# Kernel optimization log

Measured on AMD Instinct MI355X. Metric: run time of the kernel, lower is better.

## Reference

```python
import jax, jax.numpy as jnp
import numpy as np

N = 100000
F_IN = 128
HID = 128
NCLS = 40
NEG_SLOPE = 0.2
BN_EPS = 1e-5


def setup_inputs() -> dict:
    key = jax.random.key(0)
    ks = jax.random.split(key, 16)
    x = jax.random.normal(ks[0], (N, F_IN), dtype=jnp.float32)
    # self-loop-free random edges: dst = (src + 1 + r) % N
    E = 1600000
    src = jax.random.randint(ks[1], (E,), 0, N)
    off = jax.random.randint(ks[2], (E,), 1, N)
    dst = (src + off) % N
    edge_index = jnp.stack([src, dst]).astype(jnp.int64)

    def glorot(k, shape):
        fan = shape[0] + shape[-1]
        s = jnp.sqrt(6.0 / fan)
        return jax.random.uniform(k, shape, jnp.float32, -s, s)

    params = {
        'W1': glorot(ks[3], (F_IN, HID)),
        'as1': glorot(ks[4], (HID,)), 'ad1': glorot(ks[5], (HID,)),
        'b1': jnp.zeros((HID,), jnp.float32),
        'g1': jnp.ones((HID,), jnp.float32), 'beta1': jnp.zeros((HID,), jnp.float32),
        'W2': glorot(ks[6], (HID, HID)),
        'as2': glorot(ks[7], (HID,)), 'ad2': glorot(ks[8], (HID,)),
        'b2': jnp.zeros((HID,), jnp.float32),
        'g2': jnp.ones((HID,), jnp.float32), 'beta2': jnp.zeros((HID,), jnp.float32),
        'Wc': glorot(ks[9], (HID, NCLS)),
        'bc': jnp.zeros((NCLS,), jnp.float32),
    }
    return {'x': x, 'edge_index': edge_index, **params}


def _gat_conv(h_in, src, dst, W, a_src, a_dst, bias):
    # heads=1, concat=False -> single head, mean over heads is identity
    h = h_in @ W                               # [N, C]
    alpha_s = h @ a_src                        # [N]
    alpha_d = h @ a_dst                        # [N]
    alpha = alpha_s[src] + alpha_d[dst]        # [E] edge score
    alpha = jax.nn.leaky_relu(alpha, NEG_SLOPE)
    # segment softmax over destination node neighborhoods
    m = jax.ops.segment_max(alpha, dst, num_segments=N)
    e = jnp.exp(alpha - m[dst])
    s = jax.ops.segment_sum(e, dst, num_segments=N)
    alpha = e / s[dst]
    msg = h[src] * alpha[:, None]              # [E, C]
    out = jax.ops.segment_sum(msg, dst, num_segments=N)
    return out + bias


def _batchnorm(x, gamma, beta):
    mu = jnp.mean(x, axis=0)
    var = jnp.mean(jnp.square(x - mu), axis=0)  # biased, as torch BN training
    return (x - mu) * jax.lax.rsqrt(var + BN_EPS) * gamma + beta


def reference(x, edge_index, W1, as1, ad1, b1, g1, beta1,
              W2, as2, ad2, b2, g2, beta2, Wc, bc):
    src, dst = edge_index[0], edge_index[1]
    # add self loops (input edges are guaranteed self-loop-free)
    loop = jnp.arange(N, dtype=src.dtype)
    src = jnp.concatenate([src, loop])
    dst = jnp.concatenate([dst, loop])

    h = _gat_conv(x, src, dst, W1, as1, ad1, b1)
    h = jax.nn.relu(_batchnorm(h, g1, beta1))
    h = _gat_conv(h, src, dst, W2, as2, ad2, b2)
    h = jax.nn.relu(_batchnorm(h, g2, beta2))
    return h @ Wc + bc
```

## Files before the change

### kernel.cpp

```cpp
#include <hip/hip_runtime.h>
#include <hip/hip_fp16.h>
#include <math.h>


#define CDIM 128
#define NCLS_ 40
#define NEG_SLOPE_ 0.2f
#define BN_EPS_ 1e-5f
#define BRNG 256
#define BCAP 6144
#define EPB 16

using short8  = __attribute__((ext_vector_type(8))) short;
using short4v = __attribute__((ext_vector_type(4))) short;
using f32x4   = __attribute__((ext_vector_type(4))) float;

static __device__ __forceinline__ float lrelu(float a) {
    return a > 0.f ? a : NEG_SLOPE_ * a;
}
static __device__ __forceinline__ short f2bf(float f) {
    unsigned u = __float_as_uint(f);
    u += 0x7fffu + ((u >> 16) & 1u);
    return (short)(u >> 16);
}
static __device__ __forceinline__ float bf_lo(unsigned u) { return __uint_as_float(u << 16); }
static __device__ __forceinline__ float bf_hi(unsigned u) { return __uint_as_float(u & 0xffff0000u); }
static __device__ __forceinline__ __half2 u2h2(unsigned u) { return __builtin_bit_cast(__half2, u); }
static __device__ __forceinline__ unsigned h22u(__half2 h) { return __builtin_bit_cast(unsigned, h); }

__global__ void k_setup(int* bcur, float* bnsum, int NB, int n, int E, int* offs,
                        const float* __restrict__ W1, const float* __restrict__ W2,
                        const float* __restrict__ Wc,
                        short* __restrict__ Wt1, short* __restrict__ Wt2,
                        short* __restrict__ Wtc) {
    int i = blockIdx.x * blockDim.x + threadIdx.x;
    if (i < NB) bcur[i] = 0;
    if (i < 512) bnsum[i] = 0.f;
    if (i == 0) offs[n] = E + n;
    if (i < 128 * 128) {
        int k = i >> 7, nn = i & 127;
        Wt1[nn * 128 + k] = f2bf(W1[i]);
        Wt2[nn * 128 + k] = f2bf(W2[i]);
    }
    if (i < 48 * 128) {
        int nn = i >> 7, k = i & 127;
        Wtc[i] = (nn < NCLS_) ? f2bf(Wc[k * NCLS_ + nn]) : (short)0;
    }
}

__global__ __launch_bounds__(256) void k_binA(
    const int* __restrict__ src, const int* __restrict__ dst, int E,
    int* __restrict__ bcur, uint2* __restrict__ bucket, int NB)
{
    __shared__ int hist[400];
    __shared__ int base[400];
    int t = threadIdx.x;
    long e0 = (long)blockIdx.x * (256 * EPB) + t;

    for (int i = t; i < NB; i += 256) hist[i] = 0;
    __syncthreads();

    int sv[EPB], dv[EPB];
    #pragma unroll
    for (int i = 0; i < EPB; i++) {
        long e = e0 + (long)i * 256;
        if (e < E) {
            sv[i] = src[e]; dv[i] = dst[e];
            atomicAdd(&hist[dv[i] >> 8], 1);
        } else dv[i] = -1;
    }
    __syncthreads();

    for (int i = t; i < NB; i += 256) {
        int h = hist[i];
        base[i] = (h > 0) ? atomicAdd(&bcur[i], h) : 0;
    }
    __syncthreads();
    for (int i = t; i < NB; i += 256) hist[i] = 0;
    __syncthreads();

    #pragma unroll
    for (int i = 0; i < EPB; i++) {
        if (dv[i] >= 0) {
            int b = dv[i] >> 8;
            int pos = base[b] + atomicAdd(&hist[b], 1);
            if (pos < BCAP)
                bucket[(size_t)b * BCAP + pos] =
                    make_uint2((unsigned)sv[i], (unsigned)dv[i]);
        }
    }
}

__global__ __launch_bounds__(256) void k_fillB(
    const uint2* __restrict__ bucket, const int* __restrict__ bcur,
    int n, int NB, int* __restrict__ offs, int* __restrict__ csr)
{
    __shared__ int hist[256];
    __shared__ int scanb[256];
    __shared__ int cur[256];
    __shared__ int buf[BCAP + BRNG];
    int b = blockIdx.x, t = threadIdx.x;
    int node0 = b << 8;
    int nodesIn = min(BRNG, n - node0);
    int cnt = min(bcur[b], BCAP);
    const uint2* mybkt = bucket + (size_t)b * BCAP;

    int part = 0;
    for (int j = t; j < b; j += 256) part += min(bcur[j], BCAP);
    scanb[t] = part; __syncthreads();
    for (int s2 = 128; s2 > 0; s2 >>= 1) {
        if (t < s2) scanb[t] += scanb[t + s2];
        __syncthreads();
    }
    int base = scanb[0] + node0;
    __syncthreads();

    hist[t] = 0; __syncthreads();
    for (int e2 = t; e2 < cnt; e2 += 256)
        atomicAdd(&hist[mybkt[e2].y & 255], 1);
    __syncthreads();

    int v = hist[t] + ((t < nodesIn) ? 1 : 0);
    scanb[t] = v; __syncthreads();
    for (int d = 1; d < 256; d <<= 1) {
        int x2 = (t >= d) ? scanb[t - d] : 0;
        __syncthreads();
        scanb[t] += x2;
        __syncthreads();
    }
    int lo = scanb[t] - v;
    if (t < nodesIn) {
        offs[node0 + t] = base + lo;
        buf[lo] = node0 + t;
        cur[t] = lo + 1;
    }
    __syncthreads();

    for (int e2 = t; e2 < cnt; e2 += 256) {
        uint2 ed = mybkt[e2];
        int pos = atomicAdd(&cur[ed.y & 255], 1);
        buf[pos] = (int)ed.x;
    }
    __syncthreads();

    int tot = cnt + nodesIn;
    for (int j2 = t; j2 < tot; j2 += 256) csr[base + j2] = buf[j2];
}

__global__ __launch_bounds__(256) void k_gemm_mfma(
    const float* __restrict__ Xf, const unsigned* __restrict__ Xb,
    const short* __restrict__ Wt,
    const float* __restrict__ bnsum, const float* __restrict__ gamma,
    const float* __restrict__ beta, float invn,
    const float* __restrict__ av_s, const float* __restrict__ av_d,
    short* __restrict__ Hh, float* __restrict__ alpha_s, float* __restrict__ alpha_d,
    int n, int fuse)
{
    __shared__ short As[64 * 128];
    __shared__ short Bs[128 * 128];
    __shared__ float part_s[4][64];
    __shared__ float part_d[4][64];
    int t = threadIdx.x;
    int row0 = blockIdx.x * 64;

    for (int j = 0; j < 8; j++) {
        int idx = j * 256 + t;
        int nn = idx >> 4, cc = idx & 15;
        *(short8*)(Bs + nn * 128 + cc * 8) = *(const short8*)(Wt + nn * 128 + cc * 8);
    }
    float4 sc4 = make_float4(1.f, 1.f, 1.f, 1.f);
    float4 sh4 = make_float4(0.f, 0.f, 0.f, 0.f);
    if (fuse) {
        int cb = (t & 31) * 4;
        float4 s0 = *(const float4*)(bnsum + cb);
        float4 s1 = *(const float4*)(bnsum + 128 + cb);
        float4 gm = *(const float4*)(gamma + cb);
        float4 bt = *(const float4*)(beta + cb);
        float mean, var;
        mean = s0.x * invn; var = fmaxf(s1.x * invn - mean * mean, 0.f);
        sc4.x = gm.x * rsqrtf(var + BN_EPS_); sh4.x = bt.x - mean * sc4.x;
        mean = s0.y * invn; var = fmaxf(s1.y * invn - mean * mean, 0.f);
        sc4.y = gm.y * rsqrtf(var + BN_EPS_); sh4.y = bt.y - mean * sc4.y;
        mean = s0.z * invn; var = fmaxf(s1.z * invn - mean * mean, 0.f);
        sc4.z = gm.z * rsqrtf(var + BN_EPS_); sh4.z = bt.z - mean * sc4.z;
        mean = s0.w * invn; var = fmaxf(s1.w * invn - mean * mean, 0.f);
        sc4.w = gm.w * rsqrtf(var + BN_EPS_); sh4.w = bt.w - mean * sc4.w;
    }
    for (int j = 0; j < 8; j++) {
        int idx = j * 256 + t;
        int r = idx >> 5, k4 = idx & 31;
        int gr = row0 + r;
        float4 xv = make_float4(0.f, 0.f, 0.f, 0.f);
        if (fuse) {
            if (gr < n) {
                uint2 u = *(const uint2*)(Xb + (size_t)gr * 64 + k4 * 2);
                xv.x = bf_lo(u.x); xv.y = bf_hi(u.x);
                xv.z = bf_lo(u.y); xv.w = bf_hi(u.y);
            }
            xv.x = fmaxf(fmaf(xv.x, sc4.x, sh4.x), 0.f);
            xv.y = fmaxf(fmaf(xv.y, sc4.y, sh4.y), 0.f);
            xv.z = fmaxf(fmaf(xv.z, sc4.z, sh4.z), 0.f);
            xv.w = fmaxf(fmaf(xv.w, sc4.w, sh4.w), 0.f);
        } else {
            if (gr < n) xv = *(const float4*)(Xf + (size_t)gr * CDIM + k4 * 4);
        }
        short4v o;
        o.x = f2bf(xv.x); o.y = f2bf(xv.y); o.z = f2bf(xv.z); o.w = f2bf(xv.w);
        *(short4v*)(As + r * 128 + k4 * 4) = o;
    }
    __syncthreads();

    int w = t >> 6, lane = t & 63, q = lane >> 4, c = lane & 15;
    f32x4 zero = {0.f, 0.f, 0.f, 0.f};
    f32x4 acc[4][2];
    for (int i = 0; i < 4; i++) { acc[i][0] = zero; acc[i][1] = zero; }

    for (int ks = 0; ks < 4; ks++) {
        int k0 = ks * 32 + q * 8;
        short8 a0 = *(short8*)(As + (c) * 128 + k0);
        short8 a1 = *(short8*)(As + (16 + c) * 128 + k0);
        short8 a2 = *(short8*)(As + (32 + c) * 128 + k0);
        short8 a3 = *(short8*)(As + (48 + c) * 128 + k0);
        short8 b0 = *(short8*)(Bs + (w * 32 + c) * 128 + k0);
        short8 b1 = *(short8*)(Bs + (w * 32 + 16 + c) * 128 + k0);
        acc[0][0] = __builtin_amdgcn_mfma_f32_16x16x32_bf16(a0, b0, acc[0][0], 0, 0, 0);
        acc[1][0] = __builtin_amdgcn_mfma_f32_16x16x32_bf16(a1, b0, acc[1][0], 0, 0, 0);
        acc[2][0] = __builtin_amdgcn_mfma_f32_16x16x32_bf16(a2, b0, acc[2][0], 0, 0, 0);
        acc[3][0] = __builtin_amdgcn_mfma_f32_16x16x32_bf16(a3, b0, acc[3][0], 0, 0, 0);
        acc[0][1] = __builtin_amdgcn_mfma_f32_16x16x32_bf16(a0, b1, acc[0][1], 0, 0, 0);
        acc[1][1] = __builtin_amdgcn_mfma_f32_16x16x32_bf16(a1, b1, acc[1][1], 0, 0, 0);
        acc[2][1] = __builtin_amdgcn_mfma_f32_16x16x32_bf16(a2, b1, acc[2][1], 0, 0, 0);
        acc[3][1] = __builtin_amdgcn_mfma_f32_16x16x32_bf16(a3, b1, acc[3][1], 0, 0, 0);
    }

    float as0 = av_s[w * 32 + c],      as1 = av_s[w * 32 + 16 + c];
    float ad0 = av_d[w * 32 + c],      ad1 = av_d[w * 32 + 16 + c];
    #pragma unroll
    for (int mt = 0; mt < 4; mt++) {
        #pragma unroll
        for (int r = 0; r < 4; r++) {
            float v0 = acc[mt][0][r], v1 = acc[mt][1][r];
            float ps = v0 * as0 + v1 * as1;
            float pd = v0 * ad0 + v1 * ad1;
            #pragma unroll
            for (int off = 1; off < 16; off <<= 1) {
                ps += __shfl_xor(ps, off);
                pd += __shfl_xor(pd, off);
            }
            if (c == 0) {
                part_s[w][mt * 16 + q * 4 + r] = ps;
                part_d[w][mt * 16 + q * 4 + r] = pd;
            }
        }
    }
    __syncthreads();

    short* Hs = As;
    #pragma unroll
    for (int mt = 0; mt < 4; mt++)
        #pragma unroll
        for (int nt = 0; nt < 2; nt++)
            #pragma unroll
            for (int r = 0; r < 4; r++)
                Hs[(mt * 16 + q * 4 + r) * 128 + w * 32 + nt * 16 + c] =
                    (short)__half_as_ushort(__float2half_rn(acc[mt][nt][r]));

    if (t < 64) {
        int row = row0 + t;
        if (row < n) {
            alpha_s[row] = part_s[0][t] + part_s[1][t] + part_s[2][t] + part_s[3][t];
            alpha_d[row] = part_d[0][t] + part_d[1][t] + part_d[2][t] + part_d[3][t];
        }
    }
    __syncthreads();

    for (int j = 0; j < 4; j++) {
        int idx = j * 256 + t;
        int r = idx >> 4, cc = idx & 15;
        int gr = row0 + r;
        if (gr < n)
            *(short8*)(Hh + (size_t)gr * 128 + cc * 8) = *(short8*)(Hs + r * 128 + cc * 8);
    }
}

__global__ __launch_bounds__(256) void k_agg(
    const unsigned* __restrict__ Hh, const int* __restrict__ offs,
    const int* __restrict__ csr, const float* __restrict__ alpha_s,
    const float* __restrict__ alpha_d, const float* __restrict__ bias,
    unsigned* __restrict__ Ob, int n)
{
    int i = blockIdx.x * 4 + (threadIdx.x >> 6);
    int lane = threadIdx.x & 63;
    if (i >= n) return;
    int o0 = offs[i], o1 = offs[i + 1];
    float adi = alpha_d[i];

    float m = -1e30f;
    float se = 0.f;
    __half2 acc2 = __floats2half2_rn(0.f, 0.f);

    for (int c0 = o0; c0 < o1; c0 += 64) {
        int j = c0 + lane;
        int cnt = min(64, o1 - c0);
        int sj = (j < o1) ? csr[j] : 0;
        float a = (j < o1) ? lrelu(alpha_s[sj] + adi) : -1e30f;

        float cm = a;
        #pragma unroll
        for (int o = 32; o > 0; o >>= 1) cm = fmaxf(cm, __shfl_xor(cm, o));
        if (cm > m) {
            float r = __expf(m - cm);
            se *= r;
            acc2 = __hmul2(acc2, __float2half2_rn(r));
            m = cm;
        }
        float wl = (j < o1) ? __expf(a - m) : 0.f;
        se += wl;
        int wli = (int)h22u(__float2half2_rn(wl));

        for (int b = 0; b < cnt; b += 8) {
            unsigned u[8]; int wb[8];
            #pragma unroll
            for (int q2 = 0; q2 < 8; q2++) {
                int el = min(b + q2, 63);
                int s = __builtin_amdgcn_readlane(sj, el);
                wb[q2] = __builtin_amdgcn_readlane(wli, el);
                u[q2] = Hh[(size_t)(unsigned)s * 64 + lane];
            }
            #pragma unroll
            for (int q2 = 0; q2 < 8; q2++) {
                acc2 = __hfma2(u2h2(u[q2]), u2h2((unsigned)wb[q2]), acc2);
            }
        }
    }

    #pragma unroll
    for (int o = 32; o > 0; o >>= 1) se += __shfl_xor(se, o);
    float inv = 1.f / se;
    float2 af = __half22float2(acc2);
    float2 b2 = *(const float2*)(bias + lane * 2);
    float rx = fmaf(af.x, inv, b2.x);
    float ry = fmaf(af.y, inv, b2.y);
    unsigned pack = ((unsigned)(unsigned short)f2bf(ry) << 16) |
                    (unsigned)(unsigned short)f2bf(rx);
    Ob[(size_t)i * 64 + lane] = pack;
}

__global__ void k_bnstats(const unsigned* __restrict__ Hb, int n, float* __restrict__ sums) {
    __shared__ float red[4][64][4];
    int w = threadIdx.x & 63;
    int g = threadIdx.x >> 6;
    float slo = 0.f, shi = 0.f, qlo = 0.f, qhi = 0.f;
    for (int r = blockIdx.x * 4 + g; r < n; r += gridDim.x * 4) {
        unsigned u = Hb[(size_t)r * 64 + w];
        float lo = bf_lo(u), hi = bf_hi(u);
        slo += lo; shi += hi; qlo += lo * lo; qhi += hi * hi;
    }
    red[g][w][0] = slo; red[g][w][1] = shi; red[g][w][2] = qlo; red[g][w][3] = qhi;
    __syncthreads();
    if (threadIdx.x < 64) {
        int w2 = threadIdx.x;
        float s0 = 0.f, s1 = 0.f, s2 = 0.f, s3 = 0.f;
        for (int gg = 0; gg < 4; gg++) {
            s0 += red[gg][w2][0]; s1 += red[gg][w2][1];
            s2 += red[gg][w2][2]; s3 += red[gg][w2][3];
        }
        atomicAdd(&sums[2 * w2], s0);
        atomicAdd(&sums[2 * w2 + 1], s1);
        atomicAdd(&sums[128 + 2 * w2], s2);
        atomicAdd(&sums[128 + 2 * w2 + 1], s3);
    }
}

__global__ __launch_bounds__(256) void k_cls(
    const unsigned* __restrict__ G, const short* __restrict__ Wtc,
    const float* __restrict__ bc, const float* __restrict__ bnsum,
    const float* __restrict__ gamma, const float* __restrict__ beta, float invn,
    float* __restrict__ out, int n)
{
    __shared__ short As[64 * 128];
    __shared__ short Bs[48 * 128];
    int t = threadIdx.x;
    int row0 = blockIdx.x * 64;

    for (int j = 0; j < 3; j++) {
        int idx = j * 256 + t;
        *(short8*)(Bs + idx * 8) = *(const short8*)(Wtc + idx * 8);
    }
    float4 sc4, sh4;
    {
        int cb = (t & 31) * 4;
        float4 s0 = *(const float4*)(bnsum + cb);
        float4 s1 = *(const float4*)(bnsum + 128 + cb);
        float4 gm = *(const float4*)(gamma + cb);
        float4 bt = *(const float4*)(beta + cb);
        float mean, var;
        mean = s0.x * invn; var = fmaxf(s1.x * invn - mean * mean, 0.f);
        sc4.x = gm.x * rsqrtf(var + BN_EPS_); sh4.x = bt.x - mean * sc4.x;
        mean = s0.y * invn; var = fmaxf(s1.y * invn - mean * mean, 0.f);
        sc4.y = gm.y * rsqrtf(var + BN_EPS_); sh4.y = bt.y - mean * sc4.y;
        mean = s0.z * invn; var = fmaxf(s1.z * invn - mean * mean, 0.f);
        sc4.z = gm.z * rsqrtf(var + BN_EPS_); sh4.z = bt.z - mean * sc4.z;
        mean = s0.w * invn; var = fmaxf(s1.w * invn - mean * mean, 0.f);
        sc4.w = gm.w * rsqrtf(var + BN_EPS_); sh4.w = bt.w - mean * sc4.w;
    }
    for (int j = 0; j < 8; j++) {
        int idx = j * 256 + t;
        int r = idx >> 5, k4 = idx & 31;
        int gr = row0 + r;
        float4 xv = make_float4(0.f, 0.f, 0.f, 0.f);
        if (gr < n) {
            uint2 u = *(const uint2*)(G + (size_t)gr * 64 + k4 * 2);
            xv.x = bf_lo(u.x); xv.y = bf_hi(u.x);
            xv.z = bf_lo(u.y); xv.w = bf_hi(u.y);
        }
        xv.x = fmaxf(fmaf(xv.x, sc4.x, sh4.x), 0.f);
        xv.y = fmaxf(fmaf(xv.y, sc4.y, sh4.y), 0.f);
        xv.z = fmaxf(fmaf(xv.z, sc4.z, sh4.z), 0.f);
        xv.w = fmaxf(fmaf(xv.w, sc4.w, sh4.w), 0.f);
        short4v o;
        o.x = f2bf(xv.x); o.y = f2bf(xv.y); o.z = f2bf(xv.z); o.w = f2bf(xv.w);
        *(short4v*)(As + r * 128 + k4 * 4) = o;
    }
    __syncthreads();

    int w = t >> 6, lane = t & 63, q = lane >> 4, c = lane & 15;
    f32x4 zero = {0.f, 0.f, 0.f, 0.f};
    f32x4 acc[3] = {zero, zero, zero};
    for (int ks = 0; ks < 4; ks++) {
        int k0 = ks * 32 + q * 8;
        short8 a  = *(short8*)(As + (w * 16 + c) * 128 + k0);
        short8 b0 = *(short8*)(Bs + (c) * 128 + k0);
        short8 b1 = *(short8*)(Bs + (16 + c) * 128 + k0);
        short8 b2 = *(short8*)(Bs + (32 + c) * 128 + k0);
        acc[0] = __builtin_amdgcn_mfma_f32_16x16x32_bf16(a, b0, acc[0], 0, 0, 0);
        acc[1] = __builtin_amdgcn_mfma_f32_16x16x32_bf16(a, b1, acc[1], 0, 0, 0);
        acc[2] = __builtin_amdgcn_mfma_f32_16x16x32_bf16(a, b2, acc[2], 0, 0, 0);
    }
    float bc0 = bc[c], bc1 = bc[16 + c], bc2 = (c < 8) ? bc[32 + c] : 0.f;
    #pragma unroll
    for (int r = 0; r < 4; r++) {
        int row = row0 + w * 16 + q * 4 + r;
        if (row < n) {
            out[(size_t)row * NCLS_ + c]      = acc[0][r] + bc0;
            out[(size_t)row * NCLS_ + 16 + c] = acc[1][r] + bc1;
            if (c < 8) out[(size_t)row * NCLS_ + 32 + c] = acc[2][r] + bc2;
        }
    }
}

extern "C" void kernel_launch(void* const* d_in, const int* in_sizes, int n_in,
                              void* d_out, int out_size, void* d_ws, size_t ws_size,
                              hipStream_t stream)
{
    const float* x   = (const float*)d_in[0];
    const int*   ei  = (const int*)d_in[1];
    const float* W1  = (const float*)d_in[2];
    const float* as1 = (const float*)d_in[3];
    const float* ad1 = (const float*)d_in[4];
    const float* b1  = (const float*)d_in[5];
    const float* g1  = (const float*)d_in[6];
    const float* be1 = (const float*)d_in[7];
    const float* W2  = (const float*)d_in[8];
    const float* as2 = (const float*)d_in[9];
    const float* ad2 = (const float*)d_in[10];
    const float* b2  = (const float*)d_in[11];
    const float* g2  = (const float*)d_in[12];
    const float* be2 = (const float*)d_in[13];
    const float* Wc  = (const float*)d_in[14];
    const float* bc  = (const float*)d_in[15];
    float* out = (float*)d_out;

    int n = in_sizes[0] / CDIM;
    int E = in_sizes[1] / 2;
    const int* src = ei;
    const int* dst = ei + E;
    float invn = 1.f / (float)n;
    int NB = (n + BRNG - 1) / BRNG;

    char* p = (char*)d_ws;
    auto alloc = [&p](size_t bytes) { char* q = p; p += (bytes + 63) & ~(size_t)63; return q; };
    short*    Hh      = (short*)alloc((size_t)n * CDIM * sizeof(short));
    unsigned* bufB    = (unsigned*)alloc((size_t)n * 64 * sizeof(unsigned));
    float*    alpha_s = (float*)alloc((size_t)n * sizeof(float));
    float*    alpha_d = (float*)alloc((size_t)n * sizeof(float));
    float*    bnsum   = (float*)alloc(512 * sizeof(float));
    short*    Wt1     = (short*)alloc(128 * 128 * sizeof(short));
    short*    Wt2     = (short*)alloc(128 * 128 * sizeof(short));
    short*    Wtc     = (short*)alloc(48 * 128 * sizeof(short));
    int*      bcurs   = (int*)alloc((size_t)NB * sizeof(int));
    int*      offs    = (int*)alloc((size_t)(n + 1) * sizeof(int));
    uint2*    bucket  = (uint2*)alloc((size_t)NB * BCAP * sizeof(uint2));
    int*      csr     = (int*)alloc((size_t)(E + n) * sizeof(int));

    k_setup<<<dim3(64), dim3(256), 0, stream>>>(bcurs, bnsum, NB, n, E, offs,
                                                W1, W2, Wc, Wt1, Wt2, Wtc);
    k_binA<<<dim3((E + 4095) / 4096), dim3(256), 0, stream>>>(src, dst, E, bcurs, bucket, NB);
    k_fillB<<<dim3(NB), dim3(256), 0, stream>>>(bucket, bcurs, n, NB, offs, csr);

    dim3 ggrid((n + 63) / 64);
    dim3 wgrid((n + 3) / 4);

    k_gemm_mfma<<<ggrid, 256, 0, stream>>>(x, nullptr, Wt1, nullptr, nullptr, nullptr,
                                           invn, as1, ad1, Hh, alpha_s, alpha_d, n, 0);
    k_agg<<<wgrid, 256, 0, stream>>>((const unsigned*)Hh, offs, csr, alpha_s, alpha_d,
                                     b1, bufB, n);
    k_bnstats<<<dim3(256), dim3(256), 0, stream>>>(bufB, n, bnsum);

    k_gemm_mfma<<<ggrid, 256, 0, stream>>>(nullptr, bufB, Wt2, bnsum, g1, be1,
                                           invn, as2, ad2, Hh, alpha_s, alpha_d, n, 1);
    k_agg<<<wgrid, 256, 0, stream>>>((const unsigned*)Hh, offs, csr, alpha_s, alpha_d,
                                     b2, bufB, n);
    k_bnstats<<<dim3(256), dim3(256), 0, stream>>>(bufB, n, bnsum + 256);

    k_cls<<<ggrid, 256, 0, stream>>>(bufB, Wtc, bc, bnsum + 256, g2, be2, invn, out, n);
}
```

Baseline: 442.4 us.

## Prefetch neighbor feature rows in GAT aggregation with triple buffering

The attention aggregation loop now issues gathers for the first 24 neighbor rows of each 64-edge chunk before the score and max reduction. It then works through three 8-row register buffers, loading the rows 24 positions ahead while accumulating the current buffer. The aim is to hide gather latency behind the softmax arithmetic and the FMAs, instead of waiting for each batch of 8 loads before using it. In exchange it needs more vector registers, which could lower occupancy, and it may load padded rows that receive zero weight.

```diff
diff --git a/kernel.cpp b/kernel.cpp
--- a/kernel.cpp
+++ b/kernel.cpp
@@ -303,8 +303,29 @@
         int j = c0 + lane;
         int cnt = min(64, o1 - c0);
         int sj = (j < o1) ? csr[j] : 0;
+
+        unsigned ua[8], ub[8], uc[8];
+        #pragma unroll
+        for (int q = 0; q < 8; q++) {
+            int s = __builtin_amdgcn_readlane(sj, q);
+            ua[q] = Hh[(size_t)(unsigned)s * 64 + lane];
+        }
+        if (cnt > 8) {
+            #pragma unroll
+            for (int q = 0; q < 8; q++) {
+                int s = __builtin_amdgcn_readlane(sj, 8 + q);
+                ub[q] = Hh[(size_t)(unsigned)s * 64 + lane];
+            }
+        }
+        if (cnt > 16) {
+            #pragma unroll
+            for (int q = 0; q < 8; q++) {
+                int s = __builtin_amdgcn_readlane(sj, 16 + q);
+                uc[q] = Hh[(size_t)(unsigned)s * 64 + lane];
+            }
+        }
+
         float a = (j < o1) ? lrelu(alpha_s[sj] + adi) : -1e30f;
-
         float cm = a;
         #pragma unroll
         for (int o = 32; o > 0; o >>= 1) cm = fmaxf(cm, __shfl_xor(cm, o));
@@ -318,18 +339,46 @@
         se += wl;
         int wli = (int)h22u(__float2half2_rn(wl));
 
-        for (int b = 0; b < cnt; b += 8) {
-            unsigned u[8]; int wb[8];
+        for (int b = 0; b < cnt; b += 24) {
             #pragma unroll
-            for (int q2 = 0; q2 < 8; q2++) {
-                int el = min(b + q2, 63);
-                int s = __builtin_amdgcn_readlane(sj, el);
-                wb[q2] = __builtin_amdgcn_readlane(wli, el);
-                u[q2] = Hh[(size_t)(unsigned)s * 64 + lane];
-            }
-            #pragma unroll
-            for (int q2 = 0; q2 < 8; q2++) {
-                acc2 = __hfma2(u2h2(u[q2]), u2h2((unsigned)wb[q2]), acc2);
+            for (int q = 0; q < 8; q++) {
+                int wq = __builtin_amdgcn_readlane(wli, b + q);
+                acc2 = __hfma2(u2h2(ua[q]), u2h2((unsigned)wq), acc2);
+            }
+            if (b + 24 < cnt) {
+                #pragma unroll
+                for (int q = 0; q < 8; q++) {
+                    int s = __builtin_amdgcn_readlane(sj, b + 24 + q);
+                    ua[q] = Hh[(size_t)(unsigned)s * 64 + lane];
+                }
+            }
+            if (b + 8 < cnt) {
+                #pragma unroll
+                for (int q = 0; q < 8; q++) {
+                    int wq = __builtin_amdgcn_readlane(wli, b + 8 + q);
+                    acc2 = __hfma2(u2h2(ub[q]), u2h2((unsigned)wq), acc2);
+                }
+                if (b + 32 < cnt) {
+                    #pragma unroll
+                    for (int q = 0; q < 8; q++) {
+                        int s = __builtin_amdgcn_readlane(sj, b + 32 + q);
+                        ub[q] = Hh[(size_t)(unsigned)s * 64 + lane];
+                    }
+                }
+                if (b + 16 < cnt) {
+                    #pragma unroll
+                    for (int q = 0; q < 8; q++) {
+                        int wq = __builtin_amdgcn_readlane(wli, b + 16 + q);
+                        acc2 = __hfma2(u2h2(uc[q]), u2h2((unsigned)wq), acc2);
+                    }
+                    if (b + 40 < cnt) {
+                        #pragma unroll
+                        for (int q = 0; q < 8; q++) {
+                            int s = __builtin_amdgcn_readlane(sj, b + 40 + q);
+                            uc[q] = Hh[(size_t)(unsigned)s * 64 + lane];
+                        }
+                    }
+                }
             }
         }
     }
```

Result: no change. 436.0 us (-1.4%).

## Process four edges per wave with 16-byte gathers in GAT aggregation

Applied to the files above, without the earlier changes.

The aggregation kernel splits each 64-lane wave into four 16-lane groups. Each group handles a different neighbor edge and loads a 16-byte uint4 slice of the source row, where before the whole wave walked edges one at a time with 4-byte loads. The source index and fp16 softmax weight are packed into one word and distributed with ds_bpermute. Partial accumulators are combined with xor shuffles at the end, and the first 16 lanes write the output. This is meant to raise memory-level parallelism and cut per-edge loop overhead in the gather, at the cost of more registers and an extra cross-lane reduction.

```diff
diff --git a/kernel.cpp b/kernel.cpp
--- a/kernel.cpp
+++ b/kernel.cpp
@@ -26,7 +26,10 @@
 static __device__ __forceinline__ float bf_lo(unsigned u) { return __uint_as_float(u << 16); }
 static __device__ __forceinline__ float bf_hi(unsigned u) { return __uint_as_float(u & 0xffff0000u); }
 static __device__ __forceinline__ __half2 u2h2(unsigned u) { return __builtin_bit_cast(__half2, u); }
-static __device__ __forceinline__ unsigned h22u(__half2 h) { return __builtin_bit_cast(unsigned, h); }
+static __device__ __forceinline__ __half2 h2xadd(__half2 x, int mask) {
+    int o = __shfl_xor(__builtin_bit_cast(int, x), mask);
+    return __hadd2(x, __builtin_bit_cast(__half2, o));
+}
 
 __global__ void k_setup(int* bcur, float* bnsum, int NB, int n, int E, int* offs,
                         const float* __restrict__ W1, const float* __restrict__ W2,
@@ -294,16 +297,19 @@
     if (i >= n) return;
     int o0 = offs[i], o1 = offs[i + 1];
     float adi = alpha_d[i];
-
-    float m = -1e30f;
-    float se = 0.f;
-    __half2 acc2 = __floats2half2_rn(0.f, 0.f);
+    int sl = lane & 15;
+    int qa = (lane >> 4) << 2;
+    const uint4* H4 = (const uint4*)Hh;
+
+    __half2 a0h = u2h2(0), a1h = u2h2(0), a2h = u2h2(0), a3h = u2h2(0);
+    float m = -1e30f, se = 0.f;
 
     for (int c0 = o0; c0 < o1; c0 += 64) {
         int j = c0 + lane;
         int cnt = min(64, o1 - c0);
-        int sj = (j < o1) ? csr[j] : 0;
-        float a = (j < o1) ? lrelu(alpha_s[sj] + adi) : -1e30f;
+        bool v = j < o1;
+        int sj = v ? csr[j] : 0;
+        float a = v ? lrelu(alpha_s[sj] + adi) : -1e30f;
 
         float cm = a;
         #pragma unroll
@@ -311,39 +317,87 @@
         if (cm > m) {
             float r = __expf(m - cm);
             se *= r;
-            acc2 = __hmul2(acc2, __float2half2_rn(r));
+            __half2 r2 = __float2half2_rn(r);
+            a0h = __hmul2(a0h, r2); a1h = __hmul2(a1h, r2);
+            a2h = __hmul2(a2h, r2); a3h = __hmul2(a3h, r2);
             m = cm;
         }
-        float wl = (j < o1) ? __expf(a - m) : 0.f;
+        float wl = v ? __expf(a - m) : 0.f;
         se += wl;
-        int wli = (int)h22u(__float2half2_rn(wl));
-
-        for (int b = 0; b < cnt; b += 8) {
-            unsigned u[8]; int wb[8];
-            #pragma unroll
-            for (int q2 = 0; q2 < 8; q2++) {
-                int el = min(b + q2, 63);
-                int s = __builtin_amdgcn_readlane(sj, el);
-                wb[q2] = __builtin_amdgcn_readlane(wli, el);
-                u[q2] = Hh[(size_t)(unsigned)s * 64 + lane];
+        unsigned pk = ((unsigned)sj << 15) |
+                      (unsigned)__half_as_ushort(__float2half_rn(wl));
+
+        int nb = (cnt + 3) >> 2;
+        uint4 dat[8]; unsigned pkv[8];
+        #pragma unroll
+        for (int b = 0; b < 8; b++) {
+            if (b < nb) {
+                pkv[b] = (unsigned)__builtin_amdgcn_ds_bpermute(b * 16 + qa, (int)pk);
+                dat[b] = H4[(pkv[b] >> 15) * 16u + (unsigned)sl];
             }
-            #pragma unroll
-            for (int q2 = 0; q2 < 8; q2++) {
-                acc2 = __hfma2(u2h2(u[q2]), u2h2((unsigned)wb[q2]), acc2);
+        }
+        #pragma unroll
+        for (int b = 0; b < 8; b++) {
+            if (b < nb) {
+                unsigned hw = pkv[b] & 0x7fffu; hw |= hw << 16;
+                __half2 w2 = u2h2(hw);
+                a0h = __hfma2(u2h2(dat[b].x), w2, a0h);
+                a1h = __hfma2(u2h2(dat[b].y), w2, a1h);
+                a2h = __hfma2(u2h2(dat[b].z), w2, a2h);
+                a3h = __hfma2(u2h2(dat[b].w), w2, a3h);
             }
+        }
+        for (int b = 8; b < nb; b++) {
+            unsigned pv = (unsigned)__builtin_amdgcn_ds_bpermute(b * 16 + qa, (int)pk);
+            uint4 d = H4[(pv >> 15) * 16u + (unsigned)sl];
+            unsigned hw = pv & 0x7fffu; hw |= hw << 16;
+            __half2 w2 = u2h2(hw);
+            a0h = __hfma2(u2h2(d.x), w2, a0h);
+            a1h = __hfma2(u2h2(d.y), w2, a1h);
+            a2h = __hfma2(u2h2(d.z), w2, a2h);
+            a3h = __hfma2(u2h2(d.w), w2, a3h);
         }
     }
 
     #pragma unroll
     for (int o = 32; o > 0; o >>= 1) se += __shfl_xor(se, o);
     float inv = 1.f / se;
-    float2 af = __half22float2(acc2);
-    float2 b2 = *(const float2*)(bias + lane * 2);
-    float rx = fmaf(af.x, inv, b2.x);
-    float ry = fmaf(af.y, inv, b2.y);
-    unsigned pack = ((unsigned)(unsigned short)f2bf(ry) << 16) |
-                    (unsigned)(unsigned short)f2bf(rx);
-    Ob[(size_t)i * 64 + lane] = pack;
+
+    a0h = h2xadd(a0h, 32); a1h = h2xadd(a1h, 32);
+    a2h = h2xadd(a2h, 32); a3h = h2xadd(a3h, 32);
+    a0h = h2xadd(a0h, 16); a1h = h2xadd(a1h, 16);
+    a2h = h2xadd(a2h, 16); a3h = h2xadd(a3h, 16);
+
+    if (lane < 16) {
+        float2 bb0 = *(const float2*)(bias + sl * 8 + 0);
+        float2 bb1 = *(const float2*)(bias + sl * 8 + 2);
+        float2 bb2 = *(const float2*)(bias + sl * 8 + 4);
+        float2 bb3 = *(const float2*)(bias + sl * 8 + 6);
+        float2 f0 = __half22float2(a0h), f1 = __half22float2(a1h);
+        float2 f2 = __half22float2(a2h), f3 = __half22float2(a3h);
+        uint4 o4;
+        {
+            float rx = fmaf(f0.x, inv, bb0.x), ry = fmaf(f0.y, inv, bb0.y);
+            o4.x = ((unsigned)(unsigned short)f2bf(ry) << 16) |
+                   (unsigned)(unsigned short)f2bf(rx);
+        }
+        {
+            float rx = fmaf(f1.x, inv, bb1.x), ry = fmaf(f1.y, inv, bb1.y);
+            o4.y = ((unsigned)(unsigned short)f2bf(ry) << 16) |
+                   (unsigned)(unsigned short)f2bf(rx);
+        }
+        {
+            float rx = fmaf(f2.x, inv, bb2.x), ry = fmaf(f2.y, inv, bb2.y);
+            o4.z = ((unsigned)(unsigned short)f2bf(ry) << 16) |
+                   (unsigned)(unsigned short)f2bf(rx);
+        }
+        {
+            float rx = fmaf(f3.x, inv, bb3.x), ry = fmaf(f3.y, inv, bb3.y);
+            o4.w = ((unsigned)(unsigned short)f2bf(ry) << 16) |
+                   (unsigned)(unsigned short)f2bf(rx);
+        }
+        *(uint4*)(Ob + (size_t)i * 64 + sl * 4) = o4;
+    }
 }
 
 __global__ void k_bnstats(const unsigned* __restrict__ Hb, int n, float* __restrict__ sums) {
```

Result: no change. 443.5 us (+0.3%).
